# Kernel optimization log

Measured on AMD Instinct MI355X. Metric: run time of the kernel, lower is better.

## Reference

```python
import jax, jax.numpy as jnp
import numpy as np

TEMP = 0.05          # args.temp_lp_loss
NUM_CLASSES = 256

def _l2norm(x):
    return x / jnp.linalg.norm(x, axis=-1, keepdims=True)

def setup_inputs() -> dict:
    key = jax.random.key(0)
    k1, k2, k3 = jax.random.split(key, 3)
    B, C, Bs, TOPK = 2048, 2048, 4096, 4
    feats = _l2norm(jax.random.normal(k1, (B, C), jnp.float32))
    feats_s = _l2norm(jax.random.normal(k2, (Bs, TOPK, C), jnp.float32))
    labels = jax.random.randint(k3, (B,), 0, NUM_CLASSES, dtype=jnp.int32)
    # every class 0..255 appears, so each query has >=1 positive support
    labels_s = jnp.arange(Bs * TOPK, dtype=jnp.int32) % NUM_CLASSES
    return {"feats": feats, "feats_s": feats_s, "labels": labels, "labels_s": labels_s}

def reference(feats, feats_s, labels, labels_s):
    Bs, topk, C = feats_s.shape
    fs = feats_s.reshape(Bs * topk, C)                    # [N, C]
    E = jnp.exp(jnp.einsum('bc,nc->bn', feats, fs) / TEMP)  # [B, N]
    is_pos = labels[:, None] == labels_s[None, :]          # [B, N]
    # per-row hardest positive (min over positives of exp-sim)
    pos_min = jnp.min(jnp.where(is_pos, E, jnp.inf), axis=1)   # [B]
    # sum over all negatives of exp-sim
    neg_sum = jnp.sum(jnp.where(is_pos, 0.0, E), axis=1)       # [B]
    loss = -jnp.log(pos_min / (pos_min + neg_sum + 1e-6) + 1e-6)
    return jnp.mean(loss)
```

## Files before the change

### kernel.cpp

```cpp
#include <hip/hip_runtime.h>
#include <hip/hip_bf16.h>
#include <stdint.h>

#define M_TOTAL 2048
#define N_TOTAL 16384
#define K_TOTAL 2048
#define NPARTS  256

#define SCALE_E8M0 0x76767676
#define SCALE_F 512.0f

typedef __attribute__((ext_vector_type(4))) int   int4v;
typedef __attribute__((ext_vector_type(8))) int   int8v;
typedef __attribute__((ext_vector_type(4))) float floatx4;

__device__ __forceinline__ void cvt_loop(const float4* __restrict__ src,
                                         uint32_t* __restrict__ dst,
                                         int i, int stride, int n4) {
    for (; i < n4; i += stride) {
        float4 v = src[i];
        int p = __builtin_amdgcn_cvt_pk_fp8_f32(v.x * SCALE_F, v.y * SCALE_F, 0, 0);
        p = __builtin_amdgcn_cvt_pk_fp8_f32(v.z * SCALE_F, v.w * SCALE_F, p, 1);
        dst[i] = (uint32_t)p;
    }
}

__global__ void cvt_fp8_all(const float4* __restrict__ a, const float4* __restrict__ b,
                            uint32_t* __restrict__ oa, uint32_t* __restrict__ ob) {
    if (blockIdx.x < 512)
        cvt_loop(a, oa, blockIdx.x * 256 + threadIdx.x, 512 * 256,
                 M_TOTAL * K_TOTAL / 4);
    else
        cvt_loop(b, ob, (blockIdx.x - 512) * 256 + threadIdx.x, 2048 * 256,
                 N_TOTAL * K_TOTAL / 4);
}

__device__ __forceinline__ void load16(const void* g, void* l) {
    __builtin_amdgcn_global_load_lds(
        (const __attribute__((address_space(1))) void*)g,
        (__attribute__((address_space(3))) void*)l, 16, 0, 0);
}

__global__ __launch_bounds__(256) void gemm_lp(
        const char* __restrict__ Af8, const char* __restrict__ Bf8,
        const int* __restrict__ labels, const int* __restrict__ labels_s,
        float* __restrict__ pminp, float* __restrict__ psump) {
    __shared__ __align__(16) char lsA[128 * 128];
    __shared__ __align__(16) char lsB[128 * 128];
    __shared__ int lab_m[128];
    __shared__ int lab_n[128];

    const int t    = threadIdx.x;
    const int lane = t & 63;
    const int wave = t >> 6;
    const int wm   = wave >> 1;
    const int wn   = wave & 1;
    const int m0   = blockIdx.y * 128;
    const int n0   = blockIdx.x * 128;

    if (t < 128) lab_m[t] = labels[m0 + t];
    else         lab_n[t - 128] = labels_s[n0 + t - 128];

    const int rq = t >> 3;
    const int qt = (t & 7) ^ ((t >> 3) & 7);
    const char* aPtr = Af8 + (long)(m0 + rq) * K_TOTAL + qt * 16;
    const char* bPtr = Bf8 + (long)(n0 + rq) * K_TOTAL + qt * 16;
    char* lA = lsA + wave * 1024;
    char* lB = lsB + wave * 1024;

    const int quad = lane >> 4;
    const int lcol = lane & 15;
    const int plo = ((2 * quad) ^ (lcol & 7)) << 4;
    const int phi = ((2 * quad + 1) ^ (lcol & 7)) << 4;
    const char* aLo = lsA + (wm * 64 + lcol) * 128 + plo;
    const char* aHi = lsA + (wm * 64 + lcol) * 128 + phi;
    const char* bLo = lsB + (wn * 64 + lcol) * 128 + plo;
    const char* bHi = lsB + (wn * 64 + lcol) * 128 + phi;

    floatx4 acc[4][4];
#pragma unroll
    for (int mi = 0; mi < 4; ++mi)
#pragma unroll
        for (int ni = 0; ni < 4; ++ni)
            acc[mi][ni] = (floatx4){0.f, 0.f, 0.f, 0.f};

#pragma unroll 1
    for (int kt = 0; kt < K_TOTAL / 128; ++kt) {
        __syncthreads();
#pragma unroll
        for (int j = 0; j < 4; ++j) {
            load16(aPtr + j * 32 * K_TOTAL, lA + j * 4096);
            load16(bPtr + j * 32 * K_TOTAL, lB + j * 4096);
        }
        aPtr += 128;
        bPtr += 128;
        __syncthreads();

        int8v bv[4];
#pragma unroll
        for (int i = 0; i < 4; ++i) {
            int4v lo = *(const int4v*)(bLo + i * 2048);
            int4v hi = *(const int4v*)(bHi + i * 2048);
            bv[i] = (int8v){lo.x, lo.y, lo.z, lo.w, hi.x, hi.y, hi.z, hi.w};
        }
#pragma unroll
        for (int mi = 0; mi < 4; ++mi) {
            int4v lo = *(const int4v*)(aLo + mi * 2048);
            int4v hi = *(const int4v*)(aHi + mi * 2048);
            int8v av = (int8v){lo.x, lo.y, lo.z, lo.w, hi.x, hi.y, hi.z, hi.w};
#pragma unroll
            for (int ni = 0; ni < 4; ++ni)
                acc[mi][ni] = __builtin_amdgcn_mfma_scale_f32_16x16x128_f8f6f4(
                    av, bv[ni], acc[mi][ni],
                    0, 0,
                    0, SCALE_E8M0,
                    0, SCALE_E8M0);
        }
    }

    const float scale = 28.853900817779268f;
#pragma unroll
    for (int mi = 0; mi < 4; ++mi) {
#pragma unroll
        for (int r = 0; r < 4; ++r) {
            const int row_local = wm * 64 + mi * 16 + quad * 4 + r;
            const int lab = lab_m[row_local];
            float minv = __builtin_inff();
            float sumv = 0.f;
#pragma unroll
            for (int ni = 0; ni < 4; ++ni) {
                const int col_local = wn * 64 + ni * 16 + lcol;
                const float e = exp2f(acc[mi][ni][r] * scale);
                const bool pos = (lab_n[col_local] == lab);
                minv = pos ? fminf(minv, e) : minv;
                sumv = pos ? sumv : (sumv + e);
            }
#pragma unroll
            for (int off = 1; off < 16; off <<= 1) {
                minv = fminf(minv, __shfl_xor(minv, off, 16));
                sumv += __shfl_xor(sumv, off, 16);
            }
            if (lcol == 0) {
                const long idx = (long)(m0 + row_local) * NPARTS + blockIdx.x * 2 + wn;
                pminp[idx] = minv;
                psump[idx] = sumv;
            }
        }
    }
}

__global__ __launch_bounds__(256) void reduce_rows(
        const float* __restrict__ pminp, const float* __restrict__ psump,
        float* __restrict__ loss) {
    const int row  = blockIdx.x * 4 + (threadIdx.x >> 6);
    const int lane = threadIdx.x & 63;
    float m = __builtin_inff();
    float s = 0.f;
#pragma unroll
    for (int k = 0; k < NPARTS / 64; ++k) {
        const long j = (long)row * NPARTS + lane + k * 64;
        m = fminf(m, pminp[j]);
        s += psump[j];
    }
#pragma unroll
    for (int off = 1; off < 64; off <<= 1) {
        m = fminf(m, __shfl_xor(m, off, 64));
        s += __shfl_xor(s, off, 64);
    }
    if (lane == 0) loss[row] = -logf(m / (m + s + 1e-6f) + 1e-6f);
}

__global__ void final_mean(const float* __restrict__ loss, float* __restrict__ out) {
    float s = 0.f;
    for (int i = threadIdx.x; i < M_TOTAL; i += 256) s += loss[i];
#pragma unroll
    for (int off = 32; off > 0; off >>= 1) s += __shfl_xor(s, off, 64);
    __shared__ float wsum[4];
    if ((threadIdx.x & 63) == 0) wsum[threadIdx.x >> 6] = s;
    __syncthreads();
    if (threadIdx.x == 0)
        out[0] = (wsum[0] + wsum[1] + wsum[2] + wsum[3]) * (1.0f / (float)M_TOTAL);
}

extern "C" void kernel_launch(void* const* d_in, const int* in_sizes, int n_in,
                              void* d_out, int out_size, void* d_ws, size_t ws_size,
                              hipStream_t stream) {
    const float* feats    = (const float*)d_in[0];
    const float* feats_s  = (const float*)d_in[1];
    const int*   labels   = (const int*)d_in[2];
    const int*   labels_s = (const int*)d_in[3];
    float*       out      = (float*)d_out;

    char* ws = (char*)d_ws;
    char*  Af8   = ws;
    char*  Bf8   = ws + 4194304;
    float* pminp = (float*)(ws + 37748736);
    float* psump = (float*)(ws + 39845888);
    float* loss  = (float*)(ws + 41943040);

    cvt_fp8_all<<<2560, 256, 0, stream>>>((const float4*)feats, (const float4*)feats_s,
                                          (uint32_t*)Af8, (uint32_t*)Bf8);

    dim3 grid(N_TOTAL / 128, M_TOTAL / 128);
    gemm_lp<<<grid, 256, 0, stream>>>(Af8, Bf8, labels, labels_s, pminp, psump);

    reduce_rows<<<512, 256, 0, stream>>>(pminp, psump, loss);
    final_mean<<<1, 256, 0, stream>>>(loss, out);
}
```

Before: 291.2 us.

## Double-buffer 256x256 FP8 GEMM tiles with split prefetch and wider conversion stores

The GEMM tile grows from 128x128 with 4 waves to 256x256 with 8 waves, each wave computing 128x64. LDS is double-buffered, and the next K-slice is prefetched in two halves around the MFMA loop using manual waitcnt and barriers, with setprio raised during the MFMAs. The fp8 conversion kernel now packs 16 floats per thread into one uint4 store. This cuts global traffic per FLOP and hides load latency, but uses 64KB+ of LDS and 128 accumulator registers per lane, which lowers occupancy and leaves only 512 blocks.

```diff
diff --git a/kernel.cpp b/kernel.cpp
--- a/kernel.cpp
+++ b/kernel.cpp
@@ -1,11 +1,11 @@
 #include <hip/hip_runtime.h>
-#include <hip/hip_bf16.h>
 #include <stdint.h>
 
 #define M_TOTAL 2048
 #define N_TOTAL 16384
 #define K_TOTAL 2048
 #define NPARTS  256
+#define NT      (K_TOTAL / 128)
 
 #define SCALE_E8M0 0x76767676
 #define SCALE_F 512.0f
@@ -14,25 +14,35 @@
 typedef __attribute__((ext_vector_type(8))) int   int8v;
 typedef __attribute__((ext_vector_type(4))) float floatx4;
 
-__device__ __forceinline__ void cvt_loop(const float4* __restrict__ src,
-                                         uint32_t* __restrict__ dst,
-                                         int i, int stride, int n4) {
-    for (; i < n4; i += stride) {
-        float4 v = src[i];
-        int p = __builtin_amdgcn_cvt_pk_fp8_f32(v.x * SCALE_F, v.y * SCALE_F, 0, 0);
-        p = __builtin_amdgcn_cvt_pk_fp8_f32(v.z * SCALE_F, v.w * SCALE_F, p, 1);
-        dst[i] = (uint32_t)p;
-    }
-}
-
-__global__ void cvt_fp8_all(const float4* __restrict__ a, const float4* __restrict__ b,
-                            uint32_t* __restrict__ oa, uint32_t* __restrict__ ob) {
+__device__ __forceinline__ uint32_t pack8(float4 v) {
+    int p = __builtin_amdgcn_cvt_pk_fp8_f32(v.x * SCALE_F, v.y * SCALE_F, 0, 0);
+    p = __builtin_amdgcn_cvt_pk_fp8_f32(v.z * SCALE_F, v.w * SCALE_F, p, 1);
+    return (uint32_t)p;
+}
+
+__device__ __forceinline__ void cvt_loop16(const float4* __restrict__ src,
+                                           uint4* __restrict__ dst,
+                                           int i, int stride, int n16) {
+    for (; i < n16; i += stride) {
+        const float4* p = src + (size_t)i * 4;
+        uint4 o;
+        o.x = pack8(p[0]);
+        o.y = pack8(p[1]);
+        o.z = pack8(p[2]);
+        o.w = pack8(p[3]);
+        dst[i] = o;
+    }
+}
+
+__global__ __launch_bounds__(256) void cvt_fp8_all(
+        const float4* __restrict__ a, const float4* __restrict__ b,
+        uint4* __restrict__ oa, uint4* __restrict__ ob) {
     if (blockIdx.x < 512)
-        cvt_loop(a, oa, blockIdx.x * 256 + threadIdx.x, 512 * 256,
-                 M_TOTAL * K_TOTAL / 4);
+        cvt_loop16(a, oa, blockIdx.x * 256 + threadIdx.x, 512 * 256,
+                   M_TOTAL * K_TOTAL / 16);
     else
-        cvt_loop(b, ob, (blockIdx.x - 512) * 256 + threadIdx.x, 2048 * 256,
-                 N_TOTAL * K_TOTAL / 4);
+        cvt_loop16(b, ob, (blockIdx.x - 512) * 256 + threadIdx.x, 2048 * 256,
+                   N_TOTAL * K_TOTAL / 16);
 }
 
 __device__ __forceinline__ void load16(const void* g, void* l) {
@@ -41,72 +51,80 @@
         (__attribute__((address_space(3))) void*)l, 16, 0, 0);
 }
 
-__global__ __launch_bounds__(256) void gemm_lp(
+__global__ __launch_bounds__(512, 2) void gemm_lp(
         const char* __restrict__ Af8, const char* __restrict__ Bf8,
         const int* __restrict__ labels, const int* __restrict__ labels_s,
         float* __restrict__ pminp, float* __restrict__ psump) {
-    __shared__ __align__(16) char lsA[128 * 128];
-    __shared__ __align__(16) char lsB[128 * 128];
-    __shared__ int lab_m[128];
-    __shared__ int lab_n[128];
+    __shared__ __align__(16) char smA[2][256][128];
+    __shared__ __align__(16) char smB[2][256][128];
+    __shared__ int lab_m[256];
+    __shared__ int lab_n[256];
 
     const int t    = threadIdx.x;
     const int lane = t & 63;
     const int wave = t >> 6;
-    const int wm   = wave >> 1;
-    const int wn   = wave & 1;
-    const int m0   = blockIdx.y * 128;
-    const int n0   = blockIdx.x * 128;
-
-    if (t < 128) lab_m[t] = labels[m0 + t];
-    else         lab_n[t - 128] = labels_s[n0 + t - 128];
+    const int wm   = wave >> 2;
+    const int wn   = wave & 3;
+    const int m0   = blockIdx.y * 256;
+    const int n0   = blockIdx.x * 256;
+
+    if (t < 256) lab_m[t] = labels[m0 + t];
+    else         lab_n[t - 256] = labels_s[n0 + t - 256];
 
     const int rq = t >> 3;
     const int qt = (t & 7) ^ ((t >> 3) & 7);
-    const char* aPtr = Af8 + (long)(m0 + rq) * K_TOTAL + qt * 16;
-    const char* bPtr = Bf8 + (long)(n0 + rq) * K_TOTAL + qt * 16;
-    char* lA = lsA + wave * 1024;
-    char* lB = lsB + wave * 1024;
+    const char* aG = Af8 + (long)(m0 + rq) * K_TOTAL + qt * 16;
+    const char* bG = Bf8 + (long)(n0 + rq) * K_TOTAL + qt * 16;
+    const int ldst = wave * 1024;
+
+#define STAGE_A(T, J) load16(aG + (J) * 64 * K_TOTAL + (T) * 128, \
+                             &smA[(T) & 1][(J) * 64][0] + ldst)
+#define STAGE_B(T, J) load16(bG + (J) * 64 * K_TOTAL + (T) * 128, \
+                             &smB[(T) & 1][(J) * 64][0] + ldst)
 
     const int quad = lane >> 4;
     const int lcol = lane & 15;
-    const int plo = ((2 * quad) ^ (lcol & 7)) << 4;
+    const int plo = ((2 * quad)     ^ (lcol & 7)) << 4;
     const int phi = ((2 * quad + 1) ^ (lcol & 7)) << 4;
-    const char* aLo = lsA + (wm * 64 + lcol) * 128 + plo;
-    const char* aHi = lsA + (wm * 64 + lcol) * 128 + phi;
-    const char* bLo = lsB + (wn * 64 + lcol) * 128 + plo;
-    const char* bHi = lsB + (wn * 64 + lcol) * 128 + phi;
-
-    floatx4 acc[4][4];
-#pragma unroll
-    for (int mi = 0; mi < 4; ++mi)
+    const char* aF = &smA[0][wm * 128 + lcol][0];
+    const char* bF = &smB[0][wn * 64  + lcol][0];
+
+    floatx4 acc[8][4];
+#pragma unroll
+    for (int mi = 0; mi < 8; ++mi)
 #pragma unroll
         for (int ni = 0; ni < 4; ++ni)
             acc[mi][ni] = (floatx4){0.f, 0.f, 0.f, 0.f};
 
+#pragma unroll
+    for (int j = 0; j < 4; ++j) { STAGE_A(0, j); STAGE_B(0, j); }
+    STAGE_A(1, 0); STAGE_B(1, 0);
+    STAGE_A(1, 1); STAGE_B(1, 1);
+    asm volatile("s_waitcnt vmcnt(4) lgkmcnt(0)" ::: "memory");
+    __builtin_amdgcn_s_barrier();
+
 #pragma unroll 1
-    for (int kt = 0; kt < K_TOTAL / 128; ++kt) {
-        __syncthreads();
-#pragma unroll
-        for (int j = 0; j < 4; ++j) {
-            load16(aPtr + j * 32 * K_TOTAL, lA + j * 4096);
-            load16(bPtr + j * 32 * K_TOTAL, lB + j * 4096);
-        }
-        aPtr += 128;
-        bPtr += 128;
-        __syncthreads();
+    for (int kt = 0; kt < NT; ++kt) {
+        const char* aB = aF + (kt & 1) * 32768;
+        const char* bB = bF + (kt & 1) * 32768;
+
+        if (kt + 1 < NT) {
+            STAGE_A(kt + 1, 2); STAGE_B(kt + 1, 2);
+            STAGE_A(kt + 1, 3); STAGE_B(kt + 1, 3);
+        }
 
         int8v bv[4];
 #pragma unroll
-        for (int i = 0; i < 4; ++i) {
-            int4v lo = *(const int4v*)(bLo + i * 2048);
-            int4v hi = *(const int4v*)(bHi + i * 2048);
-            bv[i] = (int8v){lo.x, lo.y, lo.z, lo.w, hi.x, hi.y, hi.z, hi.w};
-        }
-#pragma unroll
-        for (int mi = 0; mi < 4; ++mi) {
-            int4v lo = *(const int4v*)(aLo + mi * 2048);
-            int4v hi = *(const int4v*)(aHi + mi * 2048);
+        for (int ni = 0; ni < 4; ++ni) {
+            int4v lo = *(const int4v*)(bB + ni * 2048 + plo);
+            int4v hi = *(const int4v*)(bB + ni * 2048 + phi);
+            bv[ni] = (int8v){lo.x, lo.y, lo.z, lo.w, hi.x, hi.y, hi.z, hi.w};
+        }
+        __builtin_amdgcn_s_setprio(1);
+#pragma unroll
+        for (int mi = 0; mi < 8; ++mi) {
+            int4v lo = *(const int4v*)(aB + mi * 2048 + plo);
+            int4v hi = *(const int4v*)(aB + mi * 2048 + phi);
             int8v av = (int8v){lo.x, lo.y, lo.z, lo.w, hi.x, hi.y, hi.z, hi.w};
 #pragma unroll
             for (int ni = 0; ni < 4; ++ni)
@@ -116,14 +134,30 @@
                     0, SCALE_E8M0,
                     0, SCALE_E8M0);
         }
-    }
+        __builtin_amdgcn_s_setprio(0);
+
+        if (kt + 1 < NT) {
+            asm volatile("s_waitcnt lgkmcnt(0)" ::: "memory");
+            __builtin_amdgcn_s_barrier();
+            if (kt + 2 < NT) {
+                STAGE_A(kt + 2, 0); STAGE_B(kt + 2, 0);
+                STAGE_A(kt + 2, 1); STAGE_B(kt + 2, 1);
+                asm volatile("s_waitcnt vmcnt(4)" ::: "memory");
+            } else {
+                asm volatile("s_waitcnt vmcnt(0)" ::: "memory");
+            }
+            __builtin_amdgcn_s_barrier();
+        }
+    }
+#undef STAGE_A
+#undef STAGE_B
 
     const float scale = 28.853900817779268f;
 #pragma unroll
-    for (int mi = 0; mi < 4; ++mi) {
+    for (int mi = 0; mi < 8; ++mi) {
 #pragma unroll
         for (int r = 0; r < 4; ++r) {
-            const int row_local = wm * 64 + mi * 16 + quad * 4 + r;
+            const int row_local = wm * 128 + mi * 16 + quad * 4 + r;
             const int lab = lab_m[row_local];
             float minv = __builtin_inff();
             float sumv = 0.f;
@@ -141,7 +175,7 @@
                 sumv += __shfl_xor(sumv, off, 16);
             }
             if (lcol == 0) {
-                const long idx = (long)(m0 + row_local) * NPARTS + blockIdx.x * 2 + wn;
+                const long idx = (long)(m0 + row_local) * NPARTS + blockIdx.x * 4 + wn;
                 pminp[idx] = minv;
                 psump[idx] = sumv;
             }
@@ -199,10 +233,10 @@
     float* loss  = (float*)(ws + 41943040);
 
     cvt_fp8_all<<<2560, 256, 0, stream>>>((const float4*)feats, (const float4*)feats_s,
-                                          (uint32_t*)Af8, (uint32_t*)Bf8);
-
-    dim3 grid(N_TOTAL / 128, M_TOTAL / 128);
-    gemm_lp<<<grid, 256, 0, stream>>>(Af8, Bf8, labels, labels_s, pminp, psump);
+                                          (uint4*)Af8, (uint4*)Bf8);
+
+    dim3 grid(N_TOTAL / 256, M_TOTAL / 256);
+    gemm_lp<<<grid, 512, 0, stream>>>(Af8, Bf8, labels, labels_s, pminp, psump);
 
     reduce_rows<<<512, 256, 0, stream>>>(pminp, psump, loss);
     final_mean<<<1, 256, 0, stream>>>(loss, out);
```

Result: slower. 303.8 us (+4.3%).

## Replace partial-buffer row reduction with global atomics and fuse loss kernels

Applied to the files above, without the earlier changes.

The GEMM epilogue now combines per-row min and sum with global atomicMin (on float bits, valid since values are non-negative) and atomicAdd instead of writing 256 partials per row. The separate reduce and mean kernels merge into a single one-block kernel, and the buffer init moves into the conversion kernel. That kernel now packs 16 fp8 values per thread and writes 16-byte stores. This removes a kernel launch and a round trip through the partials buffer, at the cost of atomic contention (256 writers per row) and a float sum whose order is no longer fixed.

```diff
diff --git a/kernel.cpp b/kernel.cpp
--- a/kernel.cpp
+++ b/kernel.cpp
@@ -5,34 +5,48 @@
 #define M_TOTAL 2048
 #define N_TOTAL 16384
 #define K_TOTAL 2048
-#define NPARTS  256
 
 #define SCALE_E8M0 0x76767676
 #define SCALE_F 512.0f
+
+#define A_U4 (M_TOTAL * K_TOTAL / 16)
+#define B_U4 (N_TOTAL * K_TOTAL / 16)
 
 typedef __attribute__((ext_vector_type(4))) int   int4v;
 typedef __attribute__((ext_vector_type(8))) int   int8v;
 typedef __attribute__((ext_vector_type(4))) float floatx4;
 
-__device__ __forceinline__ void cvt_loop(const float4* __restrict__ src,
-                                         uint32_t* __restrict__ dst,
-                                         int i, int stride, int n4) {
-    for (; i < n4; i += stride) {
-        float4 v = src[i];
-        int p = __builtin_amdgcn_cvt_pk_fp8_f32(v.x * SCALE_F, v.y * SCALE_F, 0, 0);
-        p = __builtin_amdgcn_cvt_pk_fp8_f32(v.z * SCALE_F, v.w * SCALE_F, p, 1);
-        dst[i] = (uint32_t)p;
-    }
-}
-
-__global__ void cvt_fp8_all(const float4* __restrict__ a, const float4* __restrict__ b,
-                            uint32_t* __restrict__ oa, uint32_t* __restrict__ ob) {
-    if (blockIdx.x < 512)
-        cvt_loop(a, oa, blockIdx.x * 256 + threadIdx.x, 512 * 256,
-                 M_TOTAL * K_TOTAL / 4);
-    else
-        cvt_loop(b, ob, (blockIdx.x - 512) * 256 + threadIdx.x, 2048 * 256,
-                 N_TOTAL * K_TOTAL / 4);
+__device__ __forceinline__ uint32_t pack8(float4 v) {
+    int p = __builtin_amdgcn_cvt_pk_fp8_f32(v.x * SCALE_F, v.y * SCALE_F, 0, 0);
+    p = __builtin_amdgcn_cvt_pk_fp8_f32(v.z * SCALE_F, v.w * SCALE_F, p, 1);
+    return (uint32_t)p;
+}
+
+__global__ __launch_bounds__(256) void cvt_fp8_all(
+        const float4* __restrict__ a, const float4* __restrict__ b,
+        uint4* __restrict__ oa, uint4* __restrict__ ob,
+        unsigned int* __restrict__ pminb, float* __restrict__ psumb) {
+    if (blockIdx.x == 0) {
+        for (int r = threadIdx.x; r < M_TOTAL; r += 256) {
+            pminb[r] = 0x7F800000u;
+            psumb[r] = 0.f;
+        }
+    }
+    const int stride = gridDim.x * 256;
+    for (int i = blockIdx.x * 256 + threadIdx.x; i < A_U4 + B_U4; i += stride) {
+        const float4* s;
+        uint4* d;
+        int j;
+        if (i < A_U4) { s = a; d = oa; j = i; }
+        else          { s = b; d = ob; j = i - A_U4; }
+        const float4* p = s + (size_t)j * 4;
+        uint4 o;
+        o.x = pack8(p[0]);
+        o.y = pack8(p[1]);
+        o.z = pack8(p[2]);
+        o.w = pack8(p[3]);
+        d[j] = o;
+    }
 }
 
 __device__ __forceinline__ void load16(const void* g, void* l) {
@@ -44,7 +58,7 @@
 __global__ __launch_bounds__(256) void gemm_lp(
         const char* __restrict__ Af8, const char* __restrict__ Bf8,
         const int* __restrict__ labels, const int* __restrict__ labels_s,
-        float* __restrict__ pminp, float* __restrict__ psump) {
+        unsigned int* __restrict__ pminb, float* __restrict__ psumb) {
     __shared__ __align__(16) char lsA[128 * 128];
     __shared__ __align__(16) char lsB[128 * 128];
     __shared__ int lab_m[128];
@@ -141,38 +155,23 @@
                 sumv += __shfl_xor(sumv, off, 16);
             }
             if (lcol == 0) {
-                const long idx = (long)(m0 + row_local) * NPARTS + blockIdx.x * 2 + wn;
-                pminp[idx] = minv;
-                psump[idx] = sumv;
+                const int row = m0 + row_local;
+                atomicMin(&pminb[row], __float_as_uint(minv));
+                atomicAdd(&psumb[row], sumv);
             }
         }
     }
 }
 
-__global__ __launch_bounds__(256) void reduce_rows(
-        const float* __restrict__ pminp, const float* __restrict__ psump,
-        float* __restrict__ loss) {
-    const int row  = blockIdx.x * 4 + (threadIdx.x >> 6);
-    const int lane = threadIdx.x & 63;
-    float m = __builtin_inff();
+__global__ __launch_bounds__(256) void loss_mean(
+        const unsigned int* __restrict__ pminb, const float* __restrict__ psumb,
+        float* __restrict__ out) {
     float s = 0.f;
-#pragma unroll
-    for (int k = 0; k < NPARTS / 64; ++k) {
-        const long j = (long)row * NPARTS + lane + k * 64;
-        m = fminf(m, pminp[j]);
-        s += psump[j];
-    }
-#pragma unroll
-    for (int off = 1; off < 64; off <<= 1) {
-        m = fminf(m, __shfl_xor(m, off, 64));
-        s += __shfl_xor(s, off, 64);
-    }
-    if (lane == 0) loss[row] = -logf(m / (m + s + 1e-6f) + 1e-6f);
-}
-
-__global__ void final_mean(const float* __restrict__ loss, float* __restrict__ out) {
-    float s = 0.f;
-    for (int i = threadIdx.x; i < M_TOTAL; i += 256) s += loss[i];
+    for (int r = threadIdx.x; r < M_TOTAL; r += 256) {
+        const float m = __uint_as_float(pminb[r]);
+        const float q = psumb[r];
+        s += -logf(m / (m + q + 1e-6f) + 1e-6f);
+    }
 #pragma unroll
     for (int off = 32; off > 0; off >>= 1) s += __shfl_xor(s, off, 64);
     __shared__ float wsum[4];
@@ -192,18 +191,16 @@
     float*       out      = (float*)d_out;
 
     char* ws = (char*)d_ws;
-    char*  Af8   = ws;
-    char*  Bf8   = ws + 4194304;
-    float* pminp = (float*)(ws + 37748736);
-    float* psump = (float*)(ws + 39845888);
-    float* loss  = (float*)(ws + 41943040);
+    char*         Af8   = ws;
+    char*         Bf8   = ws + 4194304;
+    unsigned int* pminb = (unsigned int*)(ws + 37748736);
+    float*        psumb = (float*)(ws + 37756928);
 
     cvt_fp8_all<<<2560, 256, 0, stream>>>((const float4*)feats, (const float4*)feats_s,
-                                          (uint32_t*)Af8, (uint32_t*)Bf8);
+                                          (uint4*)Af8, (uint4*)Bf8, pminb, psumb);
 
     dim3 grid(N_TOTAL / 128, M_TOTAL / 128);
-    gemm_lp<<<grid, 256, 0, stream>>>(Af8, Bf8, labels, labels_s, pminp, psump);
-
-    reduce_rows<<<512, 256, 0, stream>>>(pminp, psump, loss);
-    final_mean<<<1, 256, 0, stream>>>(loss, out);
-}
+    gemm_lp<<<grid, 256, 0, stream>>>(Af8, Bf8, labels, labels_s, pminb, psumb);
+
+    loss_mean<<<1, 256, 0, stream>>>(pminb, psumb, out);
+}
```

Result: slower. 357.5 us (+22.8%).
